# Kernel tuning notes

Measured on AMD Instinct MI355X. Metric: run time of the kernel, lower is better.

Reference implementation:

```python
import jax, jax.numpy as jnp
import numpy as np

D_MODEL = 1024
N_HEADS = 16


def setup_inputs() -> dict:
    key = jax.random.key(0)
    k1, k2, k3, k4, k5 = jax.random.split(key, 5)
    B, L, D = 2, 2048, D_MODEL
    scale = 1.0 / np.sqrt(D)
    return {
        "x": jax.random.normal(k1, (B, L, D), dtype=jnp.float32),
        "W_attn": jax.random.normal(k2, (D, 3 * D), dtype=jnp.float32) * scale,
        "b_attn": jax.random.normal(k3, (3 * D,), dtype=jnp.float32) * 0.02,
        "W_proj": jax.random.normal(k4, (D, D), dtype=jnp.float32) * scale,
        "b_proj": jax.random.normal(k5, (D,), dtype=jnp.float32) * 0.02,
    }


def reference(x, W_attn, b_attn, W_proj, b_proj):
    B, L, D = x.shape
    H = N_HEADS
    Dh = D // H
    qkv = x @ W_attn + b_attn  # [B, L, 3D]
    # Original torch code (faithfully reproduced bug): after splitting q,k,v,
    # q and v are overwritten with k, so q = k = v = the key projection.
    k = qkv[:, :, D:2 * D]
    kh = k.reshape(B, L, H, Dh).transpose(0, 2, 1, 3)  # [B, H, L, Dh]
    att = jnp.einsum("bhqd,bhkd->bhqk", kh, kh) / np.sqrt(Dh)
    att = jax.nn.softmax(att, axis=3)
    out = jnp.einsum("bhqk,bhkd->bhqd", att, kh)  # [B, H, L, Dh]
    out = out.transpose(0, 2, 1, 3).reshape(B, L, D)
    return out @ W_proj + b_proj
```

## Files before the change

kernel.cpp:

```cpp
#include <hip/hip_runtime.h>

#define L_SEQ 2048
#define DM    1024
#define NH    16
#define DH    64
#define BLM   4096

typedef __bf16 bf16x8 __attribute__((ext_vector_type(8)));
typedef __bf16 bf16x4 __attribute__((ext_vector_type(4)));
typedef short  s16x4  __attribute__((ext_vector_type(4)));
typedef float  f32x4  __attribute__((ext_vector_type(4)));

#define MFMA(a,b,c) __builtin_amdgcn_mfma_f32_16x16x32_bf16(a,b,c,0,0,0)

__device__ __forceinline__ f32x4 mfma16(bf16x4 a, bf16x4 b, f32x4 c) {
#if __has_builtin(__builtin_amdgcn_mfma_f32_16x16x16_bf16)
    return __builtin_amdgcn_mfma_f32_16x16x16_bf16(a, b, c, 0, 0, 0);
#elif __has_builtin(__builtin_amdgcn_mfma_f32_16x16x16bf16_1k)
    return __builtin_amdgcn_mfma_f32_16x16x16bf16_1k(
        __builtin_bit_cast(s16x4, a), __builtin_bit_cast(s16x4, b), c, 0, 0, 0);
#else
    asm("v_mfma_f32_16x16x16_bf16 %0, %1, %2, %3" : "=&v"(c) : "v"(a), "v"(b), "0"(c));
    return c;
#endif
}

__device__ __forceinline__ unsigned short f2b(float x) {
    unsigned int u = __builtin_bit_cast(unsigned int, x);
    u = (u + 0x7fffu + ((u >> 16) & 1u)) >> 16;
    return (unsigned short)u;
}

typedef __attribute__((address_space(1))) unsigned int GU32;
typedef __attribute__((address_space(3))) unsigned int LU32;
__device__ __forceinline__ void async16(const void* g, void* l) {
    __builtin_amdgcn_global_load_lds((GU32*)g, (LU32*)l, 16, 0, 0);
}

__global__ __launch_bounds__(256) void conv_x(const float* __restrict__ in,
                                              unsigned short* __restrict__ out, int n8) {
    int i = blockIdx.x * 256 + threadIdx.x;
    if (i >= n8) return;
    float4 a = ((const float4*)in)[i * 2];
    float4 b = ((const float4*)in)[i * 2 + 1];
    uint4 v;
    v.x = (unsigned)f2b(a.x) | ((unsigned)f2b(a.y) << 16);
    v.y = (unsigned)f2b(a.z) | ((unsigned)f2b(a.w) << 16);
    v.z = (unsigned)f2b(b.x) | ((unsigned)f2b(b.y) << 16);
    v.w = (unsigned)f2b(b.z) | ((unsigned)f2b(b.w) << 16);
    ((uint4*)out)[i] = v;
}

__global__ __launch_bounds__(256) void transpose_w(const float* __restrict__ W, int ld, int coff,
                                                   unsigned short* __restrict__ out) {
    __shared__ float t[32][33];
    int k0 = blockIdx.x * 32, n0 = blockIdx.y * 32;
    int tx = threadIdx.x & 31, ty = threadIdx.x >> 5;
    #pragma unroll
    for (int i = 0; i < 4; i++) {
        int k = k0 + ty + i * 8;
        t[ty + i * 8][tx] = W[(size_t)k * ld + coff + n0 + tx];
    }
    __syncthreads();
    #pragma unroll
    for (int i = 0; i < 4; i++) {
        int n = n0 + ty + i * 8;
        out[(size_t)n * DM + k0 + tx] = f2b(t[tx][ty + i * 8]);
    }
}

__global__ __launch_bounds__(256) void transpose_k(const unsigned short* __restrict__ kb,
                                                   unsigned short* __restrict__ kt) {
    __shared__ unsigned short t[64][66];
    int l0 = blockIdx.x * 64;
    int bh = blockIdx.y;
    int b = bh >> 4, h = bh & 15;
    int c = threadIdx.x & 63, r4 = threadIdx.x >> 6;
    #pragma unroll
    for (int i = 0; i < 16; i++) {
        int l = r4 + i * 4;
        t[l][c] = kb[(size_t)(b * L_SEQ + l0 + l) * DM + h * DH + c];
    }
    __syncthreads();
    const int cp = ((c >> 2) & 3) * 16 + ((c >> 4) << 2) + (c & 3);
    #pragma unroll
    for (int i = 0; i < 16; i++) {
        int d = r4 + i * 4;
        kt[(size_t)(bh * DH + d) * L_SEQ + l0 + cp] = t[c][d];
    }
}

template <int OUT_BF16>
__global__ __launch_bounds__(256) void gemm_bt(const unsigned short* __restrict__ A,
                                               const unsigned short* __restrict__ BT,
                                               const float* __restrict__ bias,
                                               void* __restrict__ Cv) {
    __shared__ __align__(16) unsigned short lA[3][64 * 64];
    __shared__ __align__(16) unsigned short lB[3][64 * 64];
    const int old = blockIdx.x + (blockIdx.y << 6);
    const int nl = (old & 7) * 128 + (old >> 3);
    const int bm = nl >> 4, bn = nl & 15;
    const int tid = threadIdx.x, wid = tid >> 6, lane = tid & 63;
    const int wr = wid >> 1, wc = wid & 1;
    const int lg = lane >> 4, lc = lane & 15;
    const int sc = (lane & 7) ^ (lane >> 3);

    f32x4 acc[2][2];
    #pragma unroll
    for (int m = 0; m < 2; m++)
        #pragma unroll
        for (int n = 0; n < 2; n++) acc[m][n] = (f32x4){0.f, 0.f, 0.f, 0.f};

    const unsigned short* gA = A + (size_t)bm * 64 * DM;
    const unsigned short* gB = BT + (size_t)bn * 64 * DM;

#define GSTAGE(buf, kk) do { \
    async16(gA + (size_t)(wid * 8 + (lane >> 3)) * DM + (kk) + sc * 8,      lA[buf] + (wid * 8) * 64 + lane * 8); \
    async16(gA + (size_t)(32 + wid * 8 + (lane >> 3)) * DM + (kk) + sc * 8, lA[buf] + (32 + wid * 8) * 64 + lane * 8); \
    async16(gB + (size_t)(wid * 8 + (lane >> 3)) * DM + (kk) + sc * 8,      lB[buf] + (wid * 8) * 64 + lane * 8); \
    async16(gB + (size_t)(32 + wid * 8 + (lane >> 3)) * DM + (kk) + sc * 8, lB[buf] + (32 + wid * 8) * 64 + lane * 8); \
} while (0)

    GSTAGE(0, 0);
    GSTAGE(1, 64);
    int cur = 0, pre = 2;
    const int NT = DM / 64;
    for (int t = 0; t < NT; ++t) {
        if (t + 1 < NT) asm volatile("s_waitcnt vmcnt(4)\n\ts_barrier" ::: "memory");
        else            asm volatile("s_waitcnt vmcnt(0)\n\ts_barrier" ::: "memory");
        if (t + 2 < NT) GSTAGE(pre, (t + 2) * 64);

        #pragma unroll
        for (int ks = 0; ks < 2; ks++) {
            bf16x8 af[2], bfv[2];
            #pragma unroll
            for (int m = 0; m < 2; m++) {
                int row = wr * 32 + m * 16 + lc;
                af[m] = *(const bf16x8*)(lA[cur] + row * 64 + ((ks * 4 + lg) ^ (lc & 7)) * 8);
            }
            #pragma unroll
            for (int n = 0; n < 2; n++) {
                int row = wc * 32 + n * 16 + lc;
                bfv[n] = *(const bf16x8*)(lB[cur] + row * 64 + ((ks * 4 + lg) ^ (lc & 7)) * 8);
            }
            #pragma unroll
            for (int m = 0; m < 2; m++)
                #pragma unroll
                for (int n = 0; n < 2; n++)
                    acc[m][n] = MFMA(af[m], bfv[n], acc[m][n]);
        }

        cur = (cur == 2) ? 0 : cur + 1;
        pre = (pre == 2) ? 0 : pre + 1;
    }
#undef GSTAGE

    #pragma unroll
    for (int m = 0; m < 2; m++) {
        int grow = bm * 64 + wr * 32 + m * 16 + lg * 4;
        #pragma unroll
        for (int n = 0; n < 2; n++) {
            int gcol = bn * 64 + wc * 32 + n * 16 + lc;
            float bs = bias[gcol];
            #pragma unroll
            for (int r = 0; r < 4; r++) {
                float v = acc[m][n][r] + bs;
                if (OUT_BF16)
                    ((unsigned short*)Cv)[(size_t)(grow + r) * DM + gcol] = f2b(v);
                else
                    ((float*)Cv)[(size_t)(grow + r) * DM + gcol] = v;
            }
        }
    }
}

__global__ __launch_bounds__(512) void attn_kernel(const unsigned short* __restrict__ kb,
                                                   const unsigned short* __restrict__ kt,
                                                   unsigned short* __restrict__ ob) {
    const int lin = blockIdx.x + (blockIdx.y << 4) + (blockIdx.z << 8);
    const int nl = (lin & 7) * 64 + (lin >> 3);
    const int qblk = nl & 15, h = (nl >> 4) & 15, b = nl >> 8;
    const int tid = threadIdx.x, wid = tid >> 6, lane = tid & 63;
    const int lg = lane >> 4, lc = lane & 15;
    const int q0 = qblk * 128 + wid * 16;
    const int bh = b * NH + h;

    __shared__ __align__(16) unsigned short kT[3][64 * 64];
    __shared__ __align__(16) unsigned short vT[3][64 * 64];

    const int srow = wid * 8 + (lane >> 3);
    const int sc = (lane & 7) ^ (srow & 7);
    const unsigned short* gK = kb + (size_t)(b * L_SEQ + srow) * DM + h * DH + sc * 8;
    const unsigned short* gV = kt + (size_t)(bh * DH + srow) * L_SEQ + sc * 8;

    bf16x8 a_q[2];
    {
        const unsigned short* base = kb + (size_t)(b * L_SEQ + q0 + lc) * DM + h * DH;
        a_q[0] = *(const bf16x8*)(base + lg * 8);
        a_q[1] = *(const bf16x8*)(base + 32 + lg * 8);
    }

    bf16x4 ones4;
    #pragma unroll
    for (int i = 0; i < 4; i++) ones4[i] = (__bf16)1.0f;

    f32x4 l_acc = (f32x4){0.f, 0.f, 0.f, 0.f};
    f32x4 o_acc[4];
    #pragma unroll
    for (int dt = 0; dt < 4; dt++) o_acc[dt] = (f32x4){0.f, 0.f, 0.f, 0.f};

    const int NT = L_SEQ / 64;
    async16(gK, &kT[0][wid * 512]);
    async16(gV, &vT[0][wid * 512]);
    async16(gK + (size_t)64 * DM, &kT[1][wid * 512]);
    async16(gV + 64,              &vT[1][wid * 512]);

    int cur = 0, pre = 2;
    for (int t = 0; t < NT; ++t) {
        if (t + 1 < NT) asm volatile("s_waitcnt vmcnt(2)\n\ts_barrier" ::: "memory");
        else            asm volatile("s_waitcnt vmcnt(0)\n\ts_barrier" ::: "memory");
        if (t + 2 < NT) {
            int k0n = (t + 2) * 64;
            async16(gK + (size_t)k0n * DM, &kT[pre][wid * 512]);
            async16(gV + k0n,              &vT[pre][wid * 512]);
        }

        f32x4 s[4];
        #pragma unroll
        for (int nt = 0; nt < 4; nt++) {
            const int r = nt * 16 + lc, x = r & 7;
            const unsigned short* kbase = &kT[cur][r * 64];
            bf16x8 k0v = *(const bf16x8*)(kbase + ((lg    ) ^ x) * 8);
            bf16x8 k1v = *(const bf16x8*)(kbase + ((lg + 4) ^ x) * 8);
            f32x4 a = (f32x4){0.f, 0.f, 0.f, 0.f};
            a = MFMA(k0v, a_q[0], a);
            s[nt] = MFMA(k1v, a_q[1], a);
        }

        bf16x4 pa[4];
        #pragma unroll
        for (int nt = 0; nt < 4; nt++)
            #pragma unroll
            for (int r = 0; r < 4; r++) {
                float p = __expf(__builtin_fmaf(s[nt][r], 0.125f, -16.0f));
                pa[nt][r] = (__bf16)p;
            }

        #pragma unroll
        for (int nt = 0; nt < 4; nt++) l_acc = mfma16(pa[nt], ones4, l_acc);

        #pragma unroll
        for (int dt = 0; dt < 4; dt++) {
            const int row = dt * 16 + lc, x = lc & 7;
            const unsigned short* vbase = &vT[cur][row * 64];
            #pragma unroll
            for (int hh = 0; hh < 2; hh++) {
                bf16x8 vb = *(const bf16x8*)(vbase + ((lg * 2 + hh) ^ x) * 8);
                bf16x4 vlo = __builtin_shufflevector(vb, vb, 0, 1, 2, 3);
                bf16x4 vhi = __builtin_shufflevector(vb, vb, 4, 5, 6, 7);
                o_acc[dt] = mfma16(pa[hh * 2],     vlo, o_acc[dt]);
                o_acc[dt] = mfma16(pa[hh * 2 + 1], vhi, o_acc[dt]);
            }
        }

        cur = (cur == 2) ? 0 : cur + 1;
        pre = (pre == 2) ? 0 : pre + 1;
    }

    #pragma unroll
    for (int r = 0; r < 4; r++) {
        float inv = 1.0f / l_acc[r];
        int row = q0 + lg * 4 + r;
        unsigned short* orow = ob + (size_t)(b * L_SEQ + row) * DM + h * DH;
        #pragma unroll
        for (int dt = 0; dt < 4; dt++)
            orow[dt * 16 + lc] = f2b(o_acc[dt][r] * inv);
    }
}

extern "C" void kernel_launch(void* const* d_in, const int* in_sizes, int n_in,
                              void* d_out, int out_size, void* d_ws, size_t ws_size,
                              hipStream_t stream) {
    (void)in_sizes; (void)n_in; (void)out_size;
    const float* x      = (const float*)d_in[0];
    const float* W_attn = (const float*)d_in[1];
    const float* b_attn = (const float*)d_in[2];
    const float* W_proj = (const float*)d_in[3];
    const float* b_proj = (const float*)d_in[4];
    float* out = (float*)d_out;

    char* ws = (char*)d_ws;
    const size_t SZ_XB = (size_t)BLM * DM * 2;
    const size_t SZ_W  = (size_t)DM * DM * 2;
    unsigned short* xb  = (unsigned short*)(ws);
    unsigned short* wkT = (unsigned short*)(ws + SZ_XB);
    unsigned short* wpT = (unsigned short*)(ws + SZ_XB + SZ_W);
    unsigned short* kbf = (unsigned short*)(ws + SZ_XB + 2 * SZ_W);
    unsigned short* ktr = (unsigned short*)(ws + 2 * SZ_XB + 2 * SZ_W);
    unsigned short* obf = (unsigned short*)(ws + 3 * SZ_XB + 2 * SZ_W);
    if (ws_size < 4 * SZ_XB + 2 * SZ_W) return;

    conv_x<<<dim3(BLM * DM / 8 / 256), dim3(256), 0, stream>>>(x, xb, BLM * DM / 8);
    transpose_w<<<dim3(32, 32), dim3(256), 0, stream>>>(W_attn, 3 * DM, DM, wkT);
    transpose_w<<<dim3(32, 32), dim3(256), 0, stream>>>(W_proj, DM, 0, wpT);
    gemm_bt<1><<<dim3(64, 16), dim3(256), 0, stream>>>(xb, wkT, b_attn + DM, (void*)kbf);
    transpose_k<<<dim3(L_SEQ / 64, 32), dim3(256), 0, stream>>>(kbf, ktr);
    attn_kernel<<<dim3(L_SEQ / 128, NH, 2), dim3(512), 0, stream>>>(kbf, ktr, obf);
    gemm_bt<0><<<dim3(64, 16), dim3(256), 0, stream>>>(obf, wpT, b_proj, out);
}
```

Before: 182.7 us.

## Enlarge GEMM M-tile to 128 and give each attention wave two query tiles

The GEMM block tile grows from 64x64 to 128x64, so each wave computes a 64x32 sub-tile and reuses B fragments across four M fragments, halving the grid. The attention kernel drops from 8 to 4 waves per block, and each wave processes 32 query rows as two 16-row tiles that share the K/V fragments loaded from LDS. Both changes aim to cut LDS and global traffic per MFMA. The cost is more accumulator registers per thread and fewer blocks and waves in flight, which can reduce latency hiding and occupancy.

```diff
diff --git a/kernel.cpp b/kernel.cpp
--- a/kernel.cpp
+++ b/kernel.cpp
@@ -95,30 +95,35 @@
                                                const unsigned short* __restrict__ BT,
                                                const float* __restrict__ bias,
                                                void* __restrict__ Cv) {
-    __shared__ __align__(16) unsigned short lA[3][64 * 64];
+    __shared__ __align__(16) unsigned short lA[3][128 * 64];
     __shared__ __align__(16) unsigned short lB[3][64 * 64];
-    const int old = blockIdx.x + (blockIdx.y << 6);
-    const int nl = (old & 7) * 128 + (old >> 3);
+    const int old = blockIdx.x + (blockIdx.y << 5);
+    const int nl = (old & 7) * 64 + (old >> 3);
     const int bm = nl >> 4, bn = nl & 15;
     const int tid = threadIdx.x, wid = tid >> 6, lane = tid & 63;
     const int wr = wid >> 1, wc = wid & 1;
     const int lg = lane >> 4, lc = lane & 15;
-    const int sc = (lane & 7) ^ (lane >> 3);
-
-    f32x4 acc[2][2];
-    #pragma unroll
-    for (int m = 0; m < 2; m++)
+    const int sr8 = lane >> 3;
+    const int sc = (lane & 7) ^ sr8;
+
+    f32x4 acc[4][2];
+    #pragma unroll
+    for (int m = 0; m < 4; m++)
         #pragma unroll
         for (int n = 0; n < 2; n++) acc[m][n] = (f32x4){0.f, 0.f, 0.f, 0.f};
 
-    const unsigned short* gA = A + (size_t)bm * 64 * DM;
+    const unsigned short* gA = A + (size_t)bm * 128 * DM;
     const unsigned short* gB = BT + (size_t)bn * 64 * DM;
 
 #define GSTAGE(buf, kk) do { \
-    async16(gA + (size_t)(wid * 8 + (lane >> 3)) * DM + (kk) + sc * 8,      lA[buf] + (wid * 8) * 64 + lane * 8); \
-    async16(gA + (size_t)(32 + wid * 8 + (lane >> 3)) * DM + (kk) + sc * 8, lA[buf] + (32 + wid * 8) * 64 + lane * 8); \
-    async16(gB + (size_t)(wid * 8 + (lane >> 3)) * DM + (kk) + sc * 8,      lB[buf] + (wid * 8) * 64 + lane * 8); \
-    async16(gB + (size_t)(32 + wid * 8 + (lane >> 3)) * DM + (kk) + sc * 8, lB[buf] + (32 + wid * 8) * 64 + lane * 8); \
+    _Pragma("unroll") \
+    for (int i = 0; i < 4; i++) \
+        async16(gA + (size_t)(wid * 32 + i * 8 + sr8) * DM + (kk) + sc * 8, \
+                lA[buf] + (wid * 32 + i * 8) * 64 + lane * 8); \
+    _Pragma("unroll") \
+    for (int i = 0; i < 2; i++) \
+        async16(gB + (size_t)(wid * 16 + i * 8 + sr8) * DM + (kk) + sc * 8, \
+                lB[buf] + (wid * 16 + i * 8) * 64 + lane * 8); \
 } while (0)
 
     GSTAGE(0, 0);
@@ -126,16 +131,16 @@
     int cur = 0, pre = 2;
     const int NT = DM / 64;
     for (int t = 0; t < NT; ++t) {
-        if (t + 1 < NT) asm volatile("s_waitcnt vmcnt(4)\n\ts_barrier" ::: "memory");
+        if (t + 1 < NT) asm volatile("s_waitcnt vmcnt(6)\n\ts_barrier" ::: "memory");
         else            asm volatile("s_waitcnt vmcnt(0)\n\ts_barrier" ::: "memory");
         if (t + 2 < NT) GSTAGE(pre, (t + 2) * 64);
 
         #pragma unroll
         for (int ks = 0; ks < 2; ks++) {
-            bf16x8 af[2], bfv[2];
-            #pragma unroll
-            for (int m = 0; m < 2; m++) {
-                int row = wr * 32 + m * 16 + lc;
+            bf16x8 af[4], bfv[2];
+            #pragma unroll
+            for (int m = 0; m < 4; m++) {
+                int row = wr * 64 + m * 16 + lc;
                 af[m] = *(const bf16x8*)(lA[cur] + row * 64 + ((ks * 4 + lg) ^ (lc & 7)) * 8);
             }
             #pragma unroll
@@ -144,7 +149,7 @@
                 bfv[n] = *(const bf16x8*)(lB[cur] + row * 64 + ((ks * 4 + lg) ^ (lc & 7)) * 8);
             }
             #pragma unroll
-            for (int m = 0; m < 2; m++)
+            for (int m = 0; m < 4; m++)
                 #pragma unroll
                 for (int n = 0; n < 2; n++)
                     acc[m][n] = MFMA(af[m], bfv[n], acc[m][n]);
@@ -156,8 +161,8 @@
 #undef GSTAGE
 
     #pragma unroll
-    for (int m = 0; m < 2; m++) {
-        int grow = bm * 64 + wr * 32 + m * 16 + lg * 4;
+    for (int m = 0; m < 4; m++) {
+        int grow = bm * 128 + wr * 64 + m * 16 + lg * 4;
         #pragma unroll
         for (int n = 0; n < 2; n++) {
             int gcol = bn * 64 + wc * 32 + n * 16 + lc;
@@ -174,7 +179,7 @@
     }
 }
 
-__global__ __launch_bounds__(512) void attn_kernel(const unsigned short* __restrict__ kb,
+__global__ __launch_bounds__(256) void attn_kernel(const unsigned short* __restrict__ kb,
                                                    const unsigned short* __restrict__ kt,
                                                    unsigned short* __restrict__ ob) {
     const int lin = blockIdx.x + (blockIdx.y << 4) + (blockIdx.z << 8);
@@ -182,72 +187,84 @@
     const int qblk = nl & 15, h = (nl >> 4) & 15, b = nl >> 8;
     const int tid = threadIdx.x, wid = tid >> 6, lane = tid & 63;
     const int lg = lane >> 4, lc = lane & 15;
-    const int q0 = qblk * 128 + wid * 16;
+    const int q0 = qblk * 128 + wid * 32;
     const int bh = b * NH + h;
 
     __shared__ __align__(16) unsigned short kT[3][64 * 64];
     __shared__ __align__(16) unsigned short vT[3][64 * 64];
 
-    const int srow = wid * 8 + (lane >> 3);
-    const int sc = (lane & 7) ^ (srow & 7);
-    const unsigned short* gK = kb + (size_t)(b * L_SEQ + srow) * DM + h * DH + sc * 8;
-    const unsigned short* gV = kt + (size_t)(bh * DH + srow) * L_SEQ + sc * 8;
-
-    bf16x8 a_q[2];
+    const int sr8 = lane >> 3;
+    const int sc = (lane & 7) ^ sr8;
+    const unsigned short* gK = kb + (size_t)b * L_SEQ * DM + h * DH;
+    const unsigned short* gV = kt + (size_t)bh * DH * L_SEQ;
+
+#define ASTAGE(buf, k0n) do { \
+    _Pragma("unroll") \
+    for (int i = 0; i < 2; i++) { \
+        int rr = wid * 16 + i * 8 + sr8; \
+        async16(gK + (size_t)((k0n) + rr) * DM + sc * 8, kT[buf] + (wid * 16 + i * 8) * 64 + lane * 8); \
+        async16(gV + (size_t)rr * L_SEQ + (k0n) + sc * 8, vT[buf] + (wid * 16 + i * 8) * 64 + lane * 8); \
+    } \
+} while (0)
+
+    bf16x8 a_q0[2], a_q1[2];
     {
         const unsigned short* base = kb + (size_t)(b * L_SEQ + q0 + lc) * DM + h * DH;
-        a_q[0] = *(const bf16x8*)(base + lg * 8);
-        a_q[1] = *(const bf16x8*)(base + 32 + lg * 8);
+        a_q0[0] = *(const bf16x8*)(base + lg * 8);
+        a_q0[1] = *(const bf16x8*)(base + 32 + lg * 8);
+        const unsigned short* base2 = base + (size_t)16 * DM;
+        a_q1[0] = *(const bf16x8*)(base2 + lg * 8);
+        a_q1[1] = *(const bf16x8*)(base2 + 32 + lg * 8);
     }
 
     bf16x4 ones4;
     #pragma unroll
     for (int i = 0; i < 4; i++) ones4[i] = (__bf16)1.0f;
 
-    f32x4 l_acc = (f32x4){0.f, 0.f, 0.f, 0.f};
-    f32x4 o_acc[4];
-    #pragma unroll
-    for (int dt = 0; dt < 4; dt++) o_acc[dt] = (f32x4){0.f, 0.f, 0.f, 0.f};
+    f32x4 l_lo = (f32x4){0.f, 0.f, 0.f, 0.f}, l_hi = l_lo;
+    f32x4 o_lo[4], o_hi[4];
+    #pragma unroll
+    for (int dt = 0; dt < 4; dt++) { o_lo[dt] = l_lo; o_hi[dt] = l_lo; }
 
     const int NT = L_SEQ / 64;
-    async16(gK, &kT[0][wid * 512]);
-    async16(gV, &vT[0][wid * 512]);
-    async16(gK + (size_t)64 * DM, &kT[1][wid * 512]);
-    async16(gV + 64,              &vT[1][wid * 512]);
+    ASTAGE(0, 0);
+    ASTAGE(1, 64);
 
     int cur = 0, pre = 2;
     for (int t = 0; t < NT; ++t) {
-        if (t + 1 < NT) asm volatile("s_waitcnt vmcnt(2)\n\ts_barrier" ::: "memory");
+        if (t + 1 < NT) asm volatile("s_waitcnt vmcnt(4)\n\ts_barrier" ::: "memory");
         else            asm volatile("s_waitcnt vmcnt(0)\n\ts_barrier" ::: "memory");
-        if (t + 2 < NT) {
-            int k0n = (t + 2) * 64;
-            async16(gK + (size_t)k0n * DM, &kT[pre][wid * 512]);
-            async16(gV + k0n,              &vT[pre][wid * 512]);
-        }
-
-        f32x4 s[4];
+        if (t + 2 < NT) ASTAGE(pre, (t + 2) * 64);
+
+        f32x4 sl[4], sh[4];
         #pragma unroll
         for (int nt = 0; nt < 4; nt++) {
-            const int r = nt * 16 + lc, x = r & 7;
+            const int r = nt * 16 + lc, x = lc & 7;
             const unsigned short* kbase = &kT[cur][r * 64];
             bf16x8 k0v = *(const bf16x8*)(kbase + ((lg    ) ^ x) * 8);
             bf16x8 k1v = *(const bf16x8*)(kbase + ((lg + 4) ^ x) * 8);
             f32x4 a = (f32x4){0.f, 0.f, 0.f, 0.f};
-            a = MFMA(k0v, a_q[0], a);
-            s[nt] = MFMA(k1v, a_q[1], a);
-        }
-
-        bf16x4 pa[4];
+            a = MFMA(k0v, a_q0[0], a);
+            sl[nt] = MFMA(k1v, a_q0[1], a);
+            f32x4 a2 = (f32x4){0.f, 0.f, 0.f, 0.f};
+            a2 = MFMA(k0v, a_q1[0], a2);
+            sh[nt] = MFMA(k1v, a_q1[1], a2);
+        }
+
+        bf16x4 pl[4], ph[4];
         #pragma unroll
         for (int nt = 0; nt < 4; nt++)
             #pragma unroll
             for (int r = 0; r < 4; r++) {
-                float p = __expf(__builtin_fmaf(s[nt][r], 0.125f, -16.0f));
-                pa[nt][r] = (__bf16)p;
-            }
-
-        #pragma unroll
-        for (int nt = 0; nt < 4; nt++) l_acc = mfma16(pa[nt], ones4, l_acc);
+                pl[nt][r] = (__bf16)__expf(__builtin_fmaf(sl[nt][r], 0.125f, -16.0f));
+                ph[nt][r] = (__bf16)__expf(__builtin_fmaf(sh[nt][r], 0.125f, -16.0f));
+            }
+
+        #pragma unroll
+        for (int nt = 0; nt < 4; nt++) {
+            l_lo = mfma16(pl[nt], ones4, l_lo);
+            l_hi = mfma16(ph[nt], ones4, l_hi);
+        }
 
         #pragma unroll
         for (int dt = 0; dt < 4; dt++) {
@@ -258,23 +275,30 @@
                 bf16x8 vb = *(const bf16x8*)(vbase + ((lg * 2 + hh) ^ x) * 8);
                 bf16x4 vlo = __builtin_shufflevector(vb, vb, 0, 1, 2, 3);
                 bf16x4 vhi = __builtin_shufflevector(vb, vb, 4, 5, 6, 7);
-                o_acc[dt] = mfma16(pa[hh * 2],     vlo, o_acc[dt]);
-                o_acc[dt] = mfma16(pa[hh * 2 + 1], vhi, o_acc[dt]);
+                o_lo[dt] = mfma16(pl[hh * 2],     vlo, o_lo[dt]);
+                o_lo[dt] = mfma16(pl[hh * 2 + 1], vhi, o_lo[dt]);
+                o_hi[dt] = mfma16(ph[hh * 2],     vlo, o_hi[dt]);
+                o_hi[dt] = mfma16(ph[hh * 2 + 1], vhi, o_hi[dt]);
             }
         }
 
         cur = (cur == 2) ? 0 : cur + 1;
         pre = (pre == 2) ? 0 : pre + 1;
     }
+#undef ASTAGE
 
     #pragma unroll
     for (int r = 0; r < 4; r++) {
-        float inv = 1.0f / l_acc[r];
-        int row = q0 + lg * 4 + r;
-        unsigned short* orow = ob + (size_t)(b * L_SEQ + row) * DM + h * DH;
-        #pragma unroll
-        for (int dt = 0; dt < 4; dt++)
-            orow[dt * 16 + lc] = f2b(o_acc[dt][r] * inv);
+        float inv_lo = 1.0f / l_lo[r];
+        float inv_hi = 1.0f / l_hi[r];
+        int row_lo = q0 + lg * 4 + r;
+        unsigned short* orow_lo = ob + (size_t)(b * L_SEQ + row_lo) * DM + h * DH;
+        unsigned short* orow_hi = orow_lo + (size_t)16 * DM;
+        #pragma unroll
+        for (int dt = 0; dt < 4; dt++) {
+            orow_lo[dt * 16 + lc] = f2b(o_lo[dt][r] * inv_lo);
+            orow_hi[dt * 16 + lc] = f2b(o_hi[dt][r] * inv_hi);
+        }
     }
 }
 
@@ -303,8 +327,8 @@
     conv_x<<<dim3(BLM * DM / 8 / 256), dim3(256), 0, stream>>>(x, xb, BLM * DM / 8);
     transpose_w<<<dim3(32, 32), dim3(256), 0, stream>>>(W_attn, 3 * DM, DM, wkT);
     transpose_w<<<dim3(32, 32), dim3(256), 0, stream>>>(W_proj, DM, 0, wpT);
-    gemm_bt<1><<<dim3(64, 16), dim3(256), 0, stream>>>(xb, wkT, b_attn + DM, (void*)kbf);
+    gemm_bt<1><<<dim3(32, 16), dim3(256), 0, stream>>>(xb, wkT, b_attn + DM, (void*)kbf);
     transpose_k<<<dim3(L_SEQ / 64, 32), dim3(256), 0, stream>>>(kbf, ktr);
-    attn_kernel<<<dim3(L_SEQ / 128, NH, 2), dim3(512), 0, stream>>>(kbf, ktr, obf);
-    gemm_bt<0><<<dim3(64, 16), dim3(256), 0, stream>>>(obf, wpT, b_proj, out);
-}
+    attn_kernel<<<dim3(16, 16, 2), dim3(256), 0, stream>>>(kbf, ktr, obf);
+    gemm_bt<0><<<dim3(32, 16), dim3(256), 0, stream>>>(obf, wpT, b_proj, out);
+}
```

After: 183.0 us. No clear change (+0.2%).
